# Kernel optimization log

Measured on AMD Instinct MI355X. Metric: run time of the kernel, lower is better.

## Reference

```python
import jax, jax.numpy as jnp
import numpy as np

B, S = 64, 200
DK = 32           # d_k = d_a = d_e
NQ = 4096         # n_question
NE = 20000        # n_exercise
NAT = 2000
NIT = 2000


def _xavier(k, shape):
    a = float(np.sqrt(6.0 / (shape[0] + shape[1])))
    return jax.random.uniform(k, shape, jnp.float32, -a, a)


def setup_inputs() -> dict:
    key = jax.random.key(0)
    ks = jax.random.split(key, 24)
    d = {}
    d['e_data'] = jax.random.randint(ks[0], (B, S), 0, NE)
    d['at_data'] = jax.random.randint(ks[1], (B, S), 0, NAT)
    d['it_data'] = jax.random.randint(ks[2], (B, S), 0, NIT)
    d['a_data'] = jax.random.randint(ks[3], (B, S), 0, 2).astype(jnp.float32)
    # binary Q-matrix: ~64 skills per exercise on average
    d['q_matrix'] = (jax.random.uniform(ks[4], (NE + 10, NQ + 1)) < (64.0 / NQ)).astype(jnp.float32)
    d['E_e'] = _xavier(ks[5], (NE + 10, DK))
    d['E_at'] = _xavier(ks[6], (NAT + 10, DK))
    d['E_it'] = _xavier(ks[7], (NIT + 10, DK))
    d['W1'] = _xavier(ks[8], (DK, 3 * DK)); d['b1'] = jnp.zeros((DK,), jnp.float32)
    d['W2'] = _xavier(ks[9], (DK, 4 * DK)); d['b2'] = jnp.zeros((DK,), jnp.float32)
    d['W3'] = _xavier(ks[10], (DK, 4 * DK)); d['b3'] = jnp.zeros((DK,), jnp.float32)
    d['W4'] = _xavier(ks[11], (DK, 3 * DK)); d['b4'] = jnp.zeros((DK,), jnp.float32)
    d['W5'] = _xavier(ks[12], (DK, 2 * DK)); d['b5'] = jnp.zeros((DK,), jnp.float32)
    d['h0'] = _xavier(ks[13], (NQ + 1, DK))
    return d


def _forward(e_data, at_data, it_data, a_data, q_matrix, E_e, E_at, E_it,
             W1, b1, W2, b2, W3, b3, W4, b4, W5, b5, h0):
    e_emb = E_e[e_data]                    # [B,S,DK]
    at_emb = E_at[at_data]                 # [B,S,DK]
    it_emb = E_it[it_data]                 # [B,S,DK]
    a_rep = jnp.broadcast_to(a_data[:, :, None], (B, S, DK))  # repeat answer to d_a
    all_learning = jnp.einsum('bsf,kf->bsk', jnp.concatenate([e_emb, at_emb, a_rep], -1), W1) + b1

    h_pre0 = jnp.broadcast_to(h0[None], (B, NQ + 1, DK))
    h_tilde0 = jnp.einsum('bn,bnd->bd', q_matrix[e_data[:, 0]], h_pre0)
    W4h, W4l, W4i = W4[:, :DK], W4[:, DK:2 * DK], W4[:, 2 * DK:]

    def step(carry, xs):
        learning_pre, h_pre, h_tilde_pre = carry
        e_t, it, learning, e_next_emb, e_next = xs
        q_e = q_matrix[e_t]                               # [B,NQ+1] gather
        x = jnp.concatenate([learning_pre, it, learning, h_tilde_pre], -1)  # [B,4DK]
        lg = jnp.tanh(x @ W2.T + b2)
        gl = jax.nn.sigmoid(x @ W3.T + b3)
        LG = gl * (lg + 1.0) * 0.5                        # [B,DK]
        LG_tilde = q_e[:, :, None] * LG[:, None, :]       # scatter (outer product), dropout off (eval)
        gamma_f = jax.nn.sigmoid(h_pre @ W4h.T + (LG @ W4l.T + it @ W4i.T + b4)[:, None, :])
        h = LG_tilde + gamma_f * h_pre                    # [B,NQ+1,DK]
        h_tilde = jnp.einsum('bn,bnd->bd', q_matrix[e_next], h)
        y = jax.nn.sigmoid(jnp.concatenate([e_next_emb, h_tilde], -1) @ W5.T + b5).sum(-1) / DK
        return (learning, h, h_tilde), y

    xs = (e_data[:, :-1].T,
          jnp.swapaxes(it_emb[:, :-1], 0, 1),
          jnp.swapaxes(all_learning[:, :-1], 0, 1),
          jnp.swapaxes(e_emb[:, 1:], 0, 1),
          e_data[:, 1:].T)
    init = (jnp.zeros((B, DK), jnp.float32), h_pre0, h_tilde0)
    _, ys = jax.lax.scan(step, init, xs)                  # ys: [S-1,B]
    pred = jnp.concatenate([jnp.zeros((B, 1), jnp.float32), ys.T], axis=1)
    return pred


def reference(e_data, at_data, it_data, a_data, q_matrix, E_e, E_at, E_it,
              W1, b1, W2, b2, W3, b3, W4, b4, W5, b5, h0):
    return _forward(e_data, at_data, it_data, a_data, q_matrix, E_e, E_at, E_it,
                    W1, b1, W2, b2, W3, b3, W4, b4, W5, b5, h0)
```

## Files before the change

### kernel.cpp

```cpp
#include <hip/hip_runtime.h>

#define Bv    64
#define Sv    200
#define DKv   32
#define NQ1v  4097
#define NWG   8
#define TPB   256
#define ROWS  2
#define NSTEP 199

typedef unsigned long long u64;

__device__ __forceinline__ float fsig(float x) {
  return __builtin_amdgcn_rcpf(1.0f + __builtin_amdgcn_exp2f(x * -1.4426950408889634f));
}
__device__ __forceinline__ float ftanh_(float x) {
  return fmaf(2.0f, fsig(2.0f * x), -1.0f);
}
__device__ __forceinline__ u64 packvt(float v, unsigned tag) {
  return ((u64)tag << 32) | (u64)__float_as_uint(v);
}
__device__ __forceinline__ u64 fresh_read(u64* p) {
  return __hip_atomic_fetch_add(p, 0ull, __ATOMIC_RELAXED, __HIP_MEMORY_SCOPE_AGENT);
}
__device__ __forceinline__ void fresh_write(u64* p, u64 v) {
  (void)__hip_atomic_exchange(p, v, __ATOMIC_RELAXED, __HIP_MEMORY_SCOPE_AGENT);
}

__global__ void lpkt_init(float* out) {
  int i = threadIdx.x;
  if (i < Bv) out[i * Sv] = 0.0f;
}

__global__ __launch_bounds__(TPB, 2) void lpkt_main(
    const int* __restrict__ e_data, const int* __restrict__ at_data,
    const int* __restrict__ it_data, const float* __restrict__ a_data,
    const float* __restrict__ q_matrix,
    const float* __restrict__ E_e, const float* __restrict__ E_at, const float* __restrict__ E_it,
    const float* __restrict__ W1, const float* __restrict__ b1,
    const float* __restrict__ W2, const float* __restrict__ b2,
    const float* __restrict__ W3, const float* __restrict__ b3,
    const float* __restrict__ W4, const float* __restrict__ b4,
    const float* __restrict__ W5, const float* __restrict__ b5,
    const float* __restrict__ h0, float* __restrict__ out,
    u64* __restrict__ partial)
{
  const int tid = threadIdx.x;
  const int wg  = blockIdx.x & (NWG - 1);
  const int b   = blockIdx.x / NWG;
  const int k   = tid & 31;
  const int p   = tid >> 5;
  const int nbase = wg * (TPB * ROWS);

  __shared__ float W23T[128 * 64];
  __shared__ __align__(16) float W1L[32 * 100];
  __shared__ __align__(16) float W4L[32 * 100];
  __shared__ __align__(16) float W5L[32 * 68];
  __shared__ float bL[5 * 32];
  __shared__ __align__(16) float xw_lds[96];
  __shared__ __align__(16) float it_lds[DKv];
  __shared__ __align__(16) float lcA[DKv], lcB[DKv];
  __shared__ __align__(16) float ht_lds[DKv];
  __shared__ __align__(16) float LG_lds[DKv];
  __shared__ __align__(16) float c_lds[DKv];
  __shared__ __align__(16) float red[8][DKv];
  __shared__ __align__(16) float red2[8][DKv];
  __shared__ float ht_part[DKv];
  __shared__ __align__(16) float h49[DKv];

  for (int idx = tid; idx < 128 * 32; idx += TPB) {
    int j = idx & 127, kk = idx >> 7;
    W23T[j * 64 + 2 * kk]     = W2[kk * 128 + j];
    W23T[j * 64 + 2 * kk + 1] = W3[kk * 128 + j];
  }
  for (int idx = tid; idx < 32 * 96; idx += TPB) {
    int r = idx / 96, c = idx % 96;
    W1L[r * 100 + c] = W1[idx];
    W4L[r * 100 + c] = W4[idx];
  }
  for (int idx = tid; idx < 32 * 64; idx += TPB) {
    int r = idx >> 6, c = idx & 63;
    W5L[r * 68 + c] = W5[idx];
  }
  if (tid < 32) {
    bL[0 * 32 + tid] = b1[tid]; bL[1 * 32 + tid] = b2[tid];
    bL[2 * 32 + tid] = b3[tid]; bL[3 * 32 + tid] = b4[tid];
    bL[4 * 32 + tid] = b5[tid];
  }
  if (tid < DKv) { ht_part[tid] = 0.0f; lcB[tid] = 0.0f; }
  if (wg == 0 && tid < DKv) h49[tid] = h0[4096 * DKv + tid];

  float h[ROWS][DKv];
#pragma unroll
  for (int r = 0; r < ROWS; r++) {
    const float4* hp = (const float4*)(h0 + (size_t)(nbase + r * TPB + tid) * DKv);
#pragma unroll
    for (int i = 0; i < 8; i++) {
      float4 v = hp[i];
      h[r][4*i] = v.x; h[r][4*i+1] = v.y; h[r][4*i+2] = v.z; h[r][4*i+3] = v.w;
    }
  }
  const int e0 = e_data[b * Sv];
  const float* q0 = q_matrix + (size_t)e0 * NQ1v;
  float qc[ROWS];
#pragma unroll
  for (int r = 0; r < ROWS; r++) qc[r] = q0[nbase + r * TPB + tid];
  float qc49 = (wg == 0 && tid < DKv) ? q0[4096] : 0.0f;
  __syncthreads();

#pragma unroll
  for (int r = 0; r < ROWS; r++) {
    if (qc[r] != 0.0f) {
#pragma unroll
      for (int kk = 0; kk < DKv; kk++) atomicAdd(&ht_part[kk], h[r][kk]);
    }
  }
  if (wg == 0 && tid < DKv && qc49 != 0.0f) atomicAdd(&ht_part[tid], h49[tid]);
  __syncthreads();
  if (tid < DKv)
    fresh_write(&partial[((size_t)(1 % 3) * Bv + b) * (NWG * DKv) + wg * DKv + tid],
                packvt(ht_part[tid], 1u));

  for (int t = 0; t < NSTEP; t++) {
    float* lc_cur  = (t & 1) ? lcB : lcA;
    float* lc_prev = (t & 1) ? lcA : lcB;
    const unsigned tau_g = (unsigned)(t + 1);
    const unsigned tau_p = (unsigned)(t + 2);

    const int ecur  = e_data[b * Sv + t];
    const int enext = e_data[b * Sv + t + 1];
    const int atc   = at_data[b * Sv + t];
    const int itc   = it_data[b * Sv + t];
    const float av  = a_data[b * Sv + t];
    const float* qnr = q_matrix + (size_t)enext * NQ1v;
    float qn[ROWS];
#pragma unroll
    for (int r = 0; r < ROWS; r++) qn[r] = qnr[nbase + r * TPB + tid];
    float qn49 = (wg == 0 && tid < DKv) ? qnr[4096] : 0.0f;

    if (tid < 96)
      xw_lds[tid] = (tid < 32) ? E_e[(size_t)ecur * DKv + tid]
                  : (tid < 64) ? E_at[(size_t)atc * DKv + (tid - 32)] : av;
    else if (tid < 128)
      it_lds[tid - 96] = E_it[(size_t)itc * DKv + (tid - 96)];

    float acc[ROWS][DKv];
#pragma unroll
    for (int kk = 0; kk < DKv; kk++) {
      float a0 = 0.0f, a1 = 0.0f;
#pragma unroll
      for (int d = 0; d < DKv; d += 4) {
        float4 w = *(const float4*)&W4[kk * 96 + d];
        a0 = fmaf(w.x, h[0][d+0], a0); a1 = fmaf(w.x, h[1][d+0], a1);
        a0 = fmaf(w.y, h[0][d+1], a0); a1 = fmaf(w.y, h[1][d+1], a1);
        a0 = fmaf(w.z, h[0][d+2], a0); a1 = fmaf(w.z, h[1][d+2], a1);
        a0 = fmaf(w.w, h[0][d+3], a0); a1 = fmaf(w.w, h[1][d+3], a1);
      }
      acc[0][kk] = a0; acc[1][kk] = a1;
    }
    __syncthreads();

    if (tid < DKv) {
      u64* pb = partial + ((size_t)(tau_g % 3) * Bv + b) * (NWG * DKv) + tid;
      u64 v[NWG];
      for (;;) {
        bool ok = true;
#pragma unroll
        for (int w2 = 0; w2 < NWG; w2++) {
          v[w2] = fresh_read(&pb[w2 * DKv]);
          ok = ok && ((unsigned)(v[w2] >> 32) == tau_g);
        }
        if (ok) break;
        __builtin_amdgcn_s_sleep(2);
      }
      float s = 0.0f;
#pragma unroll
      for (int w2 = 0; w2 < NWG; w2++) s += __uint_as_float((unsigned)v[w2]);
      ht_lds[tid] = s;
    } else if (tid >= 64 && tid < 96) {
      const int kx = tid - 64;
      float s = bL[0 * 32 + kx];
      const float4* wp = (const float4*)&W1L[kx * 100];
      const float4* xp = (const float4*)xw_lds;
#pragma unroll
      for (int i = 0; i < 24; i++) {
        float4 w = wp[i]; float4 x = xp[i];
        s = fmaf(x.x, w.x, s); s = fmaf(x.y, w.y, s);
        s = fmaf(x.z, w.z, s); s = fmaf(x.w, w.w, s);
      }
      lc_cur[kx] = s;
    }
    __syncthreads();

    {
      const int seg = p >> 1;
      const float* sp = (seg == 0) ? lc_prev : (seg == 1) ? it_lds
                      : (seg == 2) ? lc_cur  : ht_lds;
      const int off = (p & 1) * 16;
      float xv[16];
#pragma unroll
      for (int i = 0; i < 4; i++) {
        float4 v = ((const float4*)(sp + off))[i];
        xv[4*i] = v.x; xv[4*i+1] = v.y; xv[4*i+2] = v.z; xv[4*i+3] = v.w;
      }
      float s2 = 0.0f, s3 = 0.0f;
      const int jb = 16 * p;
#pragma unroll
      for (int i = 0; i < 16; i++) {
        float2 w = *(const float2*)&W23T[(jb + i) * 64 + 2 * k];
        s2 = fmaf(xv[i], w.x, s2);
        s3 = fmaf(xv[i], w.y, s3);
      }
      red[p][k] = s2; red2[p][k] = s3;
    }
    __syncthreads();

    if (tid < DKv) {
      float s2 = bL[1 * 32 + tid], s3 = bL[2 * 32 + tid];
#pragma unroll
      for (int pp = 0; pp < 8; pp++) { s2 += red[pp][tid]; s3 += red2[pp][tid]; }
      LG_lds[tid] = fsig(s3) * (ftanh_(s2) + 1.0f) * 0.5f;
    } else if (tid >= 128 && tid < 160) ht_part[tid - 128] = 0.0f;
    __syncthreads();

    {
      const float* up = (p < 4) ? (LG_lds + 8 * p) : (it_lds + 8 * (p - 4));
      const float4* wp = (const float4*)&W4L[k * 100 + 32 + 8 * p];
      float4 w0 = wp[0], w1 = wp[1];
      float pc = 0.0f;
      pc = fmaf(up[0], w0.x, pc); pc = fmaf(up[1], w0.y, pc);
      pc = fmaf(up[2], w0.z, pc); pc = fmaf(up[3], w0.w, pc);
      pc = fmaf(up[4], w1.x, pc); pc = fmaf(up[5], w1.y, pc);
      pc = fmaf(up[6], w1.z, pc); pc = fmaf(up[7], w1.w, pc);
      red[p][k] = pc;
    }
    if (wg == 0 && t >= 1 && tid >= 64 && tid < 128) {
      const int p2 = p - 2;
      const float* zs = (p2 == 0) ? xw_lds : ht_lds;
      const float4* wp = (const float4*)&W5L[k * 68 + 32 * p2];
      float acc5 = 0.0f;
#pragma unroll
      for (int i = 0; i < 8; i++) {
        float4 w = wp[i]; float4 z = ((const float4*)zs)[i];
        acc5 = fmaf(z.x, w.x, acc5); acc5 = fmaf(z.y, w.y, acc5);
        acc5 = fmaf(z.z, w.z, acc5); acc5 = fmaf(z.w, w.w, acc5);
      }
      red2[p2][k] = acc5;
    }
    __syncthreads();

    if (tid < DKv) {
      float s = bL[3 * 32 + tid];
#pragma unroll
      for (int pp = 0; pp < 8; pp++) s += red[pp][tid];
      c_lds[tid] = s;
    } else if (wg == 0 && t >= 1 && tid >= 96 && tid < 128) {
      const int kx = tid - 96;
      float s = fsig(bL[4 * 32 + kx] + red2[0][kx] + red2[1][kx]);
#pragma unroll
      for (int m = 1; m < 32; m <<= 1) s += __shfl_xor(s, m);
      if (tid == 96) out[b * Sv + t] = s * (1.0f / DKv);
    }
    __syncthreads();

    {
      float c_r[DKv], lg_r[DKv];
#pragma unroll
      for (int i = 0; i < 8; i++) {
        float4 cv = ((const float4*)c_lds)[i];
        float4 gv = ((const float4*)LG_lds)[i];
        c_r[4*i] = cv.x; c_r[4*i+1] = cv.y; c_r[4*i+2] = cv.z; c_r[4*i+3] = cv.w;
        lg_r[4*i] = gv.x; lg_r[4*i+1] = gv.y; lg_r[4*i+2] = gv.z; lg_r[4*i+3] = gv.w;
      }
#pragma unroll
      for (int r = 0; r < ROWS; r++) {
        const float qcr = qc[r];
#pragma unroll
        for (int kk = 0; kk < DKv; kk++) {
          float g = fsig(acc[r][kk] + c_r[kk]);
          h[r][kk] = fmaf(g, h[r][kk], qcr * lg_r[kk]);
        }
        if (qn[r] != 0.0f) {
#pragma unroll
          for (int kk = 0; kk < DKv; kk++) atomicAdd(&ht_part[kk], h[r][kk]);
        }
        qc[r] = qn[r];
      }
    }
    if (wg == 0 && tid < DKv) {
      float hh[DKv];
#pragma unroll
      for (int i = 0; i < 8; i++) {
        float4 v = ((const float4*)h49)[i];
        hh[4*i] = v.x; hh[4*i+1] = v.y; hh[4*i+2] = v.z; hh[4*i+3] = v.w;
      }
      float a = c_lds[tid];
#pragma unroll
      for (int d = 0; d < DKv; d += 4) {
        float4 w = *(const float4*)&W4L[tid * 100 + d];
        a = fmaf(w.x, hh[d+0], a); a = fmaf(w.y, hh[d+1], a);
        a = fmaf(w.z, hh[d+2], a); a = fmaf(w.w, hh[d+3], a);
      }
      float hn = fmaf(fsig(a), h49[tid], qc49 * LG_lds[tid]);
      h49[tid] = hn;
      if (qn49 != 0.0f) atomicAdd(&ht_part[tid], hn);
      qc49 = qn49;
    }
    __syncthreads();

    if (tid < DKv)
      fresh_write(&partial[((size_t)(tau_p % 3) * Bv + b) * (NWG * DKv) + wg * DKv + tid],
                  packvt(ht_part[tid], tau_p));
  }

  if (wg == 0) {
    const unsigned tau_f = (unsigned)(NSTEP + 1);
    if (tid < DKv) {
      u64* pb = partial + ((size_t)(tau_f % 3) * Bv + b) * (NWG * DKv) + tid;
      u64 v[NWG];
      for (;;) {
        bool ok = true;
#pragma unroll
        for (int w2 = 0; w2 < NWG; w2++) {
          v[w2] = fresh_read(&pb[w2 * DKv]);
          ok = ok && ((unsigned)(v[w2] >> 32) == tau_f);
        }
        if (ok) break;
        __builtin_amdgcn_s_sleep(2);
      }
      float s = 0.0f;
#pragma unroll
      for (int w2 = 0; w2 < NWG; w2++) s += __uint_as_float((unsigned)v[w2]);
      ht_lds[tid] = s;
      xw_lds[tid] = E_e[(size_t)e_data[b * Sv + 199] * DKv + tid];
    }
    __syncthreads();
    if (tid >= 64 && tid < 128) {
      const int p2 = p - 2;
      const float* zs = (p2 == 0) ? xw_lds : ht_lds;
      const float4* wp = (const float4*)&W5L[k * 68 + 32 * p2];
      float acc5 = 0.0f;
#pragma unroll
      for (int i = 0; i < 8; i++) {
        float4 w = wp[i]; float4 z = ((const float4*)zs)[i];
        acc5 = fmaf(z.x, w.x, acc5); acc5 = fmaf(z.y, w.y, acc5);
        acc5 = fmaf(z.z, w.z, acc5); acc5 = fmaf(z.w, w.w, acc5);
      }
      red2[p2][k] = acc5;
    }
    __syncthreads();
    if (tid >= 96 && tid < 128) {
      const int kx = tid - 96;
      float s = fsig(bL[4 * 32 + kx] + red2[0][kx] + red2[1][kx]);
#pragma unroll
      for (int m = 1; m < 32; m <<= 1) s += __shfl_xor(s, m);
      if (tid == 96) out[b * Sv + 199] = s * (1.0f / DKv);
    }
  }
}

extern "C" void kernel_launch(void* const* d_in, const int* in_sizes, int n_in,
                              void* d_out, int out_size, void* d_ws, size_t ws_size,
                              hipStream_t stream) {
  const int*   e_data   = (const int*)d_in[0];
  const int*   at_data  = (const int*)d_in[1];
  const int*   it_data  = (const int*)d_in[2];
  const float* a_data   = (const float*)d_in[3];
  const float* q_matrix = (const float*)d_in[4];
  const float* E_e      = (const float*)d_in[5];
  const float* E_at     = (const float*)d_in[6];
  const float* E_it     = (const float*)d_in[7];
  const float* W1 = (const float*)d_in[8];
  const float* b1 = (const float*)d_in[9];
  const float* W2 = (const float*)d_in[10];
  const float* b2 = (const float*)d_in[11];
  const float* W3 = (const float*)d_in[12];
  const float* b3 = (const float*)d_in[13];
  const float* W4 = (const float*)d_in[14];
  const float* b4 = (const float*)d_in[15];
  const float* W5 = (const float*)d_in[16];
  const float* b5 = (const float*)d_in[17];
  const float* h0 = (const float*)d_in[18];
  float* out = (float*)d_out;

  u64* partial = (u64*)d_ws;

  lpkt_init<<<1, 64, 0, stream>>>(out);
  lpkt_main<<<dim3(Bv * NWG), dim3(TPB), 0, stream>>>(
      e_data, at_data, it_data, a_data, q_matrix, E_e, E_at, E_it,
      W1, b1, W2, b2, W3, b3, W4, b4, W5, b5, h0, out, partial);
}
```

Baseline: 4.910 ms.

## Collapse per-step small matvecs into one wavefront and defer non-contributing row updates

The W2/W3 gate matvec, the W4 learning/interval projection and the W5 prediction head each ran spread across all 8 wavefronts, with LDS reductions and several block barriers per step. They now run inside the first 64 threads using transposed weight tables, with a cross-lane shuffle pairing the W2 and W3 results, which removes three barriers per timestep. Rows that feed the next step's h_tilde are updated before the partial sums are published to other workgroups. Rows that do not contribute are updated after the publish, shortening the critical path of the cross-workgroup chain. The cost is serial 128-long dot products per thread on one wavefront and divergent row-update branches.

```diff
diff --git a/kernel.cpp b/kernel.cpp
--- a/kernel.cpp
+++ b/kernel.cpp
@@ -48,14 +48,14 @@
   const int tid = threadIdx.x;
   const int wg  = blockIdx.x & (NWG - 1);
   const int b   = blockIdx.x / NWG;
-  const int k   = tid & 31;
-  const int p   = tid >> 5;
   const int nbase = wg * (TPB * ROWS);
 
-  __shared__ float W23T[128 * 64];
+  __shared__ float W2T[128 * 32];
+  __shared__ float W3T[128 * 32];
   __shared__ __align__(16) float W1L[32 * 100];
   __shared__ __align__(16) float W4L[32 * 100];
-  __shared__ __align__(16) float W5L[32 * 68];
+  __shared__ float W4xT[64 * 32];
+  __shared__ float W5T[64 * 32];
   __shared__ float bL[5 * 32];
   __shared__ __align__(16) float xw_lds[96];
   __shared__ __align__(16) float it_lds[DKv];
@@ -63,15 +63,13 @@
   __shared__ __align__(16) float ht_lds[DKv];
   __shared__ __align__(16) float LG_lds[DKv];
   __shared__ __align__(16) float c_lds[DKv];
-  __shared__ __align__(16) float red[8][DKv];
-  __shared__ __align__(16) float red2[8][DKv];
   __shared__ float ht_part[DKv];
   __shared__ __align__(16) float h49[DKv];
 
   for (int idx = tid; idx < 128 * 32; idx += TPB) {
-    int j = idx & 127, kk = idx >> 7;
-    W23T[j * 64 + 2 * kk]     = W2[kk * 128 + j];
-    W23T[j * 64 + 2 * kk + 1] = W3[kk * 128 + j];
+    int kk = idx >> 7, f = idx & 127;
+    W2T[f * 32 + kk] = W2[idx];
+    W3T[f * 32 + kk] = W3[idx];
   }
   for (int idx = tid; idx < 32 * 96; idx += TPB) {
     int r = idx / 96, c = idx % 96;
@@ -79,8 +77,9 @@
     W4L[r * 100 + c] = W4[idx];
   }
   for (int idx = tid; idx < 32 * 64; idx += TPB) {
-    int r = idx >> 6, c = idx & 63;
-    W5L[r * 68 + c] = W5[idx];
+    int j = idx >> 6, f = idx & 63;
+    W4xT[f * 32 + j] = W4[j * 96 + 32 + f];
+    W5T[f * 32 + j]  = W5[j * 64 + f];
   }
   if (tid < 32) {
     bL[0 * 32 + tid] = b1[tid]; bL[1 * 32 + tid] = b2[tid];
@@ -189,102 +188,93 @@
         s = fmaf(x.z, w.z, s); s = fmaf(x.w, w.w, s);
       }
       lc_cur[kx] = s;
-    }
-    __syncthreads();
-
-    {
-      const int seg = p >> 1;
-      const float* sp = (seg == 0) ? lc_prev : (seg == 1) ? it_lds
-                      : (seg == 2) ? lc_cur  : ht_lds;
-      const int off = (p & 1) * 16;
-      float xv[16];
-#pragma unroll
-      for (int i = 0; i < 4; i++) {
-        float4 v = ((const float4*)(sp + off))[i];
-        xv[4*i] = v.x; xv[4*i+1] = v.y; xv[4*i+2] = v.z; xv[4*i+3] = v.w;
-      }
-      float s2 = 0.0f, s3 = 0.0f;
-      const int jb = 16 * p;
-#pragma unroll
-      for (int i = 0; i < 16; i++) {
-        float2 w = *(const float2*)&W23T[(jb + i) * 64 + 2 * k];
-        s2 = fmaf(xv[i], w.x, s2);
-        s3 = fmaf(xv[i], w.y, s3);
-      }
-      red[p][k] = s2; red2[p][k] = s3;
-    }
-    __syncthreads();
-
-    if (tid < DKv) {
-      float s2 = bL[1 * 32 + tid], s3 = bL[2 * 32 + tid];
-#pragma unroll
-      for (int pp = 0; pp < 8; pp++) { s2 += red[pp][tid]; s3 += red2[pp][tid]; }
-      LG_lds[tid] = fsig(s3) * (ftanh_(s2) + 1.0f) * 0.5f;
-    } else if (tid >= 128 && tid < 160) ht_part[tid - 128] = 0.0f;
-    __syncthreads();
-
-    {
-      const float* up = (p < 4) ? (LG_lds + 8 * p) : (it_lds + 8 * (p - 4));
-      const float4* wp = (const float4*)&W4L[k * 100 + 32 + 8 * p];
-      float4 w0 = wp[0], w1 = wp[1];
-      float pc = 0.0f;
-      pc = fmaf(up[0], w0.x, pc); pc = fmaf(up[1], w0.y, pc);
-      pc = fmaf(up[2], w0.z, pc); pc = fmaf(up[3], w0.w, pc);
-      pc = fmaf(up[4], w1.x, pc); pc = fmaf(up[5], w1.y, pc);
-      pc = fmaf(up[6], w1.z, pc); pc = fmaf(up[7], w1.w, pc);
-      red[p][k] = pc;
-    }
-    if (wg == 0 && t >= 1 && tid >= 64 && tid < 128) {
-      const int p2 = p - 2;
-      const float* zs = (p2 == 0) ? xw_lds : ht_lds;
-      const float4* wp = (const float4*)&W5L[k * 68 + 32 * p2];
-      float acc5 = 0.0f;
-#pragma unroll
-      for (int i = 0; i < 8; i++) {
-        float4 w = wp[i]; float4 z = ((const float4*)zs)[i];
-        acc5 = fmaf(z.x, w.x, acc5); acc5 = fmaf(z.y, w.y, acc5);
-        acc5 = fmaf(z.z, w.z, acc5); acc5 = fmaf(z.w, w.w, acc5);
-      }
-      red2[p2][k] = acc5;
-    }
-    __syncthreads();
-
-    if (tid < DKv) {
-      float s = bL[3 * 32 + tid];
-#pragma unroll
-      for (int pp = 0; pp < 8; pp++) s += red[pp][tid];
-      c_lds[tid] = s;
-    } else if (wg == 0 && t >= 1 && tid >= 96 && tid < 128) {
-      const int kx = tid - 96;
-      float s = fsig(bL[4 * 32 + kx] + red2[0][kx] + red2[1][kx]);
-#pragma unroll
-      for (int m = 1; m < 32; m <<= 1) s += __shfl_xor(s, m);
-      if (tid == 96) out[b * Sv + t] = s * (1.0f / DKv);
-    }
-    __syncthreads();
-
-    {
-      float c_r[DKv], lg_r[DKv];
-#pragma unroll
-      for (int i = 0; i < 8; i++) {
-        float4 cv = ((const float4*)c_lds)[i];
-        float4 gv = ((const float4*)LG_lds)[i];
-        c_r[4*i] = cv.x; c_r[4*i+1] = cv.y; c_r[4*i+2] = cv.z; c_r[4*i+3] = cv.w;
-        lg_r[4*i] = gv.x; lg_r[4*i+1] = gv.y; lg_r[4*i+2] = gv.z; lg_r[4*i+3] = gv.w;
-      }
-#pragma unroll
-      for (int r = 0; r < ROWS; r++) {
+    } else if (tid >= 128 && tid < 160) {
+      ht_part[tid - 128] = 0.0f;
+    }
+    __syncthreads();
+
+    if (tid < 64) {
+      const int j = tid & 31;
+      const float* Wt = (tid < 32) ? W2T : W3T;
+      float sa = (tid < 32) ? bL[1 * 32 + j] : bL[2 * 32 + j];
+      float sb = 0.0f;
+#pragma unroll
+      for (int f = 0; f < 32; f += 2) {
+        sa = fmaf(lc_prev[f],     Wt[(f    ) * 32 + j], sa);
+        sb = fmaf(lc_prev[f + 1], Wt[(f + 1) * 32 + j], sb);
+      }
+#pragma unroll
+      for (int f = 0; f < 32; f += 2) {
+        sa = fmaf(it_lds[f],     Wt[(32 + f    ) * 32 + j], sa);
+        sb = fmaf(it_lds[f + 1], Wt[(32 + f + 1) * 32 + j], sb);
+      }
+#pragma unroll
+      for (int f = 0; f < 32; f += 2) {
+        sa = fmaf(lc_cur[f],     Wt[(64 + f    ) * 32 + j], sa);
+        sb = fmaf(lc_cur[f + 1], Wt[(64 + f + 1) * 32 + j], sb);
+      }
+#pragma unroll
+      for (int f = 0; f < 32; f += 2) {
+        sa = fmaf(ht_lds[f],     Wt[(96 + f    ) * 32 + j], sa);
+        sb = fmaf(ht_lds[f + 1], Wt[(96 + f + 1) * 32 + j], sb);
+      }
+      const float s = sa + sb;
+      const float cross = __shfl_xor(s, 32);
+      if (tid < 32) {
+        LG_lds[j] = fsig(cross) * (ftanh_(s) + 1.0f) * 0.5f;
+      }
+      if (tid < 32) {
+        float s4a = bL[3 * 32 + j], s4b = 0.0f;
+#pragma unroll
+        for (int f = 0; f < 32; f += 2) {
+          s4a = fmaf(LG_lds[f],     W4xT[(f    ) * 32 + j], s4a);
+          s4b = fmaf(LG_lds[f + 1], W4xT[(f + 1) * 32 + j], s4b);
+        }
+#pragma unroll
+        for (int f = 0; f < 32; f += 2) {
+          s4a = fmaf(it_lds[f],     W4xT[(32 + f    ) * 32 + j], s4a);
+          s4b = fmaf(it_lds[f + 1], W4xT[(32 + f + 1) * 32 + j], s4b);
+        }
+        c_lds[j] = s4a + s4b;
+      } else if (wg == 0 && t >= 1) {
+        float s5a = bL[4 * 32 + j], s5b = 0.0f;
+#pragma unroll
+        for (int f = 0; f < 32; f += 2) {
+          s5a = fmaf(xw_lds[f],     W5T[(f    ) * 32 + j], s5a);
+          s5b = fmaf(xw_lds[f + 1], W5T[(f + 1) * 32 + j], s5b);
+        }
+#pragma unroll
+        for (int f = 0; f < 32; f += 2) {
+          s5a = fmaf(ht_lds[f],     W5T[(32 + f    ) * 32 + j], s5a);
+          s5b = fmaf(ht_lds[f + 1], W5T[(32 + f + 1) * 32 + j], s5b);
+        }
+        float yv = fsig(s5a + s5b);
+#pragma unroll
+        for (int m = 1; m < 32; m <<= 1) yv += __shfl_xor(yv, m);
+        if (j == 0) out[b * Sv + t] = yv * (1.0f / DKv);
+      }
+    }
+    __syncthreads();
+
+    float c_r[DKv], lg_r[DKv];
+#pragma unroll
+    for (int i = 0; i < 8; i++) {
+      float4 cv = ((const float4*)c_lds)[i];
+      float4 gv = ((const float4*)LG_lds)[i];
+      c_r[4*i] = cv.x; c_r[4*i+1] = cv.y; c_r[4*i+2] = cv.z; c_r[4*i+3] = cv.w;
+      lg_r[4*i] = gv.x; lg_r[4*i+1] = gv.y; lg_r[4*i+2] = gv.z; lg_r[4*i+3] = gv.w;
+    }
+#pragma unroll
+    for (int r = 0; r < ROWS; r++) {
+      if (qn[r] != 0.0f) {
         const float qcr = qc[r];
 #pragma unroll
         for (int kk = 0; kk < DKv; kk++) {
           float g = fsig(acc[r][kk] + c_r[kk]);
           h[r][kk] = fmaf(g, h[r][kk], qcr * lg_r[kk]);
         }
-        if (qn[r] != 0.0f) {
-#pragma unroll
-          for (int kk = 0; kk < DKv; kk++) atomicAdd(&ht_part[kk], h[r][kk]);
-        }
-        qc[r] = qn[r];
+#pragma unroll
+        for (int kk = 0; kk < DKv; kk++) atomicAdd(&ht_part[kk], h[r][kk]);
       }
     }
     if (wg == 0 && tid < DKv) {
@@ -294,7 +284,7 @@
         float4 v = ((const float4*)h49)[i];
         hh[4*i] = v.x; hh[4*i+1] = v.y; hh[4*i+2] = v.z; hh[4*i+3] = v.w;
       }
-      float a = c_lds[tid];
+      float a = c_r[0] * 0.0f + c_lds[tid];
 #pragma unroll
       for (int d = 0; d < DKv; d += 4) {
         float4 w = *(const float4*)&W4L[tid * 100 + d];
@@ -304,13 +294,26 @@
       float hn = fmaf(fsig(a), h49[tid], qc49 * LG_lds[tid]);
       h49[tid] = hn;
       if (qn49 != 0.0f) atomicAdd(&ht_part[tid], hn);
-      qc49 = qn49;
-    }
+    }
+    qc49 = qn49;
     __syncthreads();
 
     if (tid < DKv)
       fresh_write(&partial[((size_t)(tau_p % 3) * Bv + b) * (NWG * DKv) + wg * DKv + tid],
                   packvt(ht_part[tid], tau_p));
+
+#pragma unroll
+    for (int r = 0; r < ROWS; r++) {
+      if (qn[r] == 0.0f) {
+        const float qcr = qc[r];
+#pragma unroll
+        for (int kk = 0; kk < DKv; kk++) {
+          float g = fsig(acc[r][kk] + c_r[kk]);
+          h[r][kk] = fmaf(g, h[r][kk], qcr * lg_r[kk]);
+        }
+      }
+      qc[r] = qn[r];
+    }
   }
 
   if (wg == 0) {
@@ -335,26 +338,22 @@
       xw_lds[tid] = E_e[(size_t)e_data[b * Sv + 199] * DKv + tid];
     }
     __syncthreads();
-    if (tid >= 64 && tid < 128) {
-      const int p2 = p - 2;
-      const float* zs = (p2 == 0) ? xw_lds : ht_lds;
-      const float4* wp = (const float4*)&W5L[k * 68 + 32 * p2];
-      float acc5 = 0.0f;
-#pragma unroll
-      for (int i = 0; i < 8; i++) {
-        float4 w = wp[i]; float4 z = ((const float4*)zs)[i];
-        acc5 = fmaf(z.x, w.x, acc5); acc5 = fmaf(z.y, w.y, acc5);
-        acc5 = fmaf(z.z, w.z, acc5); acc5 = fmaf(z.w, w.w, acc5);
-      }
-      red2[p2][k] = acc5;
-    }
-    __syncthreads();
-    if (tid >= 96 && tid < 128) {
-      const int kx = tid - 96;
-      float s = fsig(bL[4 * 32 + kx] + red2[0][kx] + red2[1][kx]);
-#pragma unroll
-      for (int m = 1; m < 32; m <<= 1) s += __shfl_xor(s, m);
-      if (tid == 96) out[b * Sv + 199] = s * (1.0f / DKv);
+    if (tid < 32) {
+      float s5a = bL[4 * 32 + tid], s5b = 0.0f;
+#pragma unroll
+      for (int f = 0; f < 32; f += 2) {
+        s5a = fmaf(xw_lds[f],     W5T[(f    ) * 32 + tid], s5a);
+        s5b = fmaf(xw_lds[f + 1], W5T[(f + 1) * 32 + tid], s5b);
+      }
+#pragma unroll
+      for (int f = 0; f < 32; f += 2) {
+        s5a = fmaf(ht_lds[f],     W5T[(32 + f    ) * 32 + tid], s5a);
+        s5b = fmaf(ht_lds[f + 1], W5T[(32 + f + 1) * 32 + tid], s5b);
+      }
+      float yv = fsig(s5a + s5b);
+#pragma unroll
+      for (int m = 1; m < 32; m <<= 1) yv += __shfl_xor(yv, m);
+      if (tid == 0) out[b * Sv + 199] = yv * (1.0f / DKv);
     }
   }
 }
```

Result: slower. 6.404 ms (+30.4%).
